# Optimization experiments

Measured on AMD Instinct MI355X. Metric: run time of the kernel, lower is better.

The kernel has to match this reference:

```python
import jax, jax.numpy as jnp
import numpy as np

NUM_GRAPHS = 256
LAMBDA = 0.01


def setup_inputs() -> dict:
    key = jax.random.key(0)
    k1, k2, k3, k4, k5 = jax.random.split(key, 5)
    N, D, E = 100000, 64, 1200000
    logits = jax.random.normal(k1, (NUM_GRAPHS, 10), dtype=jnp.float32)
    labels = jax.random.randint(k2, (NUM_GRAPHS,), 0, 10, dtype=jnp.int64)
    x = jax.random.normal(k3, (N, D), dtype=jnp.float32)
    edge_index = jax.random.randint(k4, (2, E), 0, N, dtype=jnp.int64)
    batch = jnp.sort(jax.random.randint(k5, (N,), 0, NUM_GRAPHS, dtype=jnp.int64))
    return {"logits": logits, "labels": labels, "x": x,
            "edge_index": edge_index, "batch": batch}


def reference(logits, labels, x, edge_index, batch):
    # cross-entropy (mean over graphs)
    logp = jax.nn.log_softmax(logits, axis=-1)
    ce_loss = -jnp.mean(jnp.take_along_axis(logp, labels[:, None], axis=1))

    # Dirichlet energy
    row, col = edge_index[0], edge_index[1]
    N = x.shape[0]
    ones_e = jnp.ones(row.shape, dtype=x.dtype)
    deg = jax.ops.segment_sum(ones_e, row, num_segments=N)          # [N]
    deg_inv_sqrt = jnp.where(deg > 0, jax.lax.rsqrt(jnp.where(deg > 0, deg, 1.0)), 0.0)
    norm = deg_inv_sqrt[row] * deg_inv_sqrt[col]                    # [E]
    diff = x[row] - x[col]                                          # [E, D]
    sq = jnp.sum(diff * diff, axis=1)                               # [E]
    energy_e = norm * sq

    seg = batch[row]                                                # graph id per edge
    energy_sum = jax.ops.segment_sum(energy_e, seg, num_segments=NUM_GRAPHS)
    edge_counts = jax.ops.segment_sum(ones_e, seg, num_segments=NUM_GRAPHS)
    edge_counts = jnp.clip(edge_counts, 1.0, None)
    smoothness_loss = jnp.mean(energy_sum / edge_counts)

    return ce_loss + LAMBDA * smoothness_loss
```

## Files before the change

kernel.cpp:

```cpp
#include <hip/hip_runtime.h>
#include <math.h>

#define NUM_GRAPHS 256
#define LAMBDA 0.01f

typedef int            v4i __attribute__((ext_vector_type(4)));
typedef float          v4f __attribute__((ext_vector_type(4)));
typedef unsigned int   v4u __attribute__((ext_vector_type(4)));
typedef unsigned short v8h __attribute__((ext_vector_type(8)));

__device__ __forceinline__ unsigned short f2bf_rne(float f) {
    unsigned int u = __float_as_uint(f);
    u = u + 0x7fffu + ((u >> 16) & 1u);
    return (unsigned short)(u >> 16);
}

__device__ __forceinline__ float bfdiff_sq(v4u a, v4u b) {
    float s = 0.0f;
    #pragma unroll
    for (int k = 0; k < 4; ++k) {
        float alo = __uint_as_float(a[k] << 16);
        float ahi = __uint_as_float(a[k] & 0xffff0000u);
        float blo = __uint_as_float(b[k] << 16);
        float bhi = __uint_as_float(b[k] & 0xffff0000u);
        float d1 = alo - blo;
        float d2 = ahi - bhi;
        s += d1 * d1;
        s += d2 * d2;
    }
    return s;
}

__global__ void k_cvt(const float* __restrict__ x, v8h* __restrict__ xh,
                      float* __restrict__ zr, int zcount8, long total8) {
    long j = (long)blockIdx.x * blockDim.x + threadIdx.x;
    if (j < total8) {
        const v4f* xp = (const v4f*)(x + j * 8);
        v4f a = xp[0], b = xp[1];
        v8h o;
        o[0] = f2bf_rne(a[0]); o[1] = f2bf_rne(a[1]);
        o[2] = f2bf_rne(a[2]); o[3] = f2bf_rne(a[3]);
        o[4] = f2bf_rne(b[0]); o[5] = f2bf_rne(b[1]);
        o[6] = f2bf_rne(b[2]); o[7] = f2bf_rne(b[3]);
        __builtin_nontemporal_store(o, xh + j);
    }
    if (j < zcount8) {
        v4f z = {0.0f, 0.0f, 0.0f, 0.0f};
        v4f* zp = (v4f*)(zr + j * 8);
        zp[0] = z; zp[1] = z;
    }
}

__global__ void __launch_bounds__(256, 4)
k_gather(const int* __restrict__ row, const int* __restrict__ col,
         const v4u* __restrict__ xh4, float* __restrict__ deg,
         float* __restrict__ sq, int E) {
    const int lane   = threadIdx.x & 63;
    const int lane8  = lane & 7;
    const int gi     = lane >> 3;
    const int wave   = (blockIdx.x * blockDim.x + threadIdx.x) >> 6;
    const int nwaves = (gridDim.x * blockDim.x) >> 6;
    const int E64    = E >> 6;

    for (int t = wave; t < E64; t += nwaves) {
        const int ebase = t * 64 + gi * 8;

        v4i rv0 = __builtin_nontemporal_load((const v4i*)(row + ebase));
        v4i rv1 = __builtin_nontemporal_load((const v4i*)(row + ebase + 4));
        v4i cv0 = __builtin_nontemporal_load((const v4i*)(col + ebase));
        v4i cv1 = __builtin_nontemporal_load((const v4i*)(col + ebase + 4));

        v4u a0 = xh4[(long)rv0[0] * 8 + lane8];
        v4u b0 = xh4[(long)cv0[0] * 8 + lane8];
        v4u a1 = xh4[(long)rv0[1] * 8 + lane8];
        v4u b1 = xh4[(long)cv0[1] * 8 + lane8];
        v4u a2 = xh4[(long)rv0[2] * 8 + lane8];
        v4u b2 = xh4[(long)cv0[2] * 8 + lane8];
        v4u a3 = xh4[(long)rv0[3] * 8 + lane8];
        v4u b3 = xh4[(long)cv0[3] * 8 + lane8];
        v4u a4 = xh4[(long)rv1[0] * 8 + lane8];
        v4u b4 = xh4[(long)cv1[0] * 8 + lane8];
        v4u a5 = xh4[(long)rv1[1] * 8 + lane8];
        v4u b5 = xh4[(long)cv1[1] * 8 + lane8];
        v4u a6 = xh4[(long)rv1[2] * 8 + lane8];
        v4u b6 = xh4[(long)cv1[2] * 8 + lane8];
        v4u a7 = xh4[(long)rv1[3] * 8 + lane8];
        v4u b7 = xh4[(long)cv1[3] * 8 + lane8];

        float s0 = bfdiff_sq(a0, b0);
        float s1 = bfdiff_sq(a1, b1);
        float s2 = bfdiff_sq(a2, b2);
        float s3 = bfdiff_sq(a3, b3);
        float s4 = bfdiff_sq(a4, b4);
        float s5 = bfdiff_sq(a5, b5);
        float s6 = bfdiff_sq(a6, b6);
        float s7 = bfdiff_sq(a7, b7);

        s0 += __shfl_xor(s0, 1); s1 += __shfl_xor(s1, 1);
        s2 += __shfl_xor(s2, 1); s3 += __shfl_xor(s3, 1);
        s4 += __shfl_xor(s4, 1); s5 += __shfl_xor(s5, 1);
        s6 += __shfl_xor(s6, 1); s7 += __shfl_xor(s7, 1);
        s0 += __shfl_xor(s0, 2); s1 += __shfl_xor(s1, 2);
        s2 += __shfl_xor(s2, 2); s3 += __shfl_xor(s3, 2);
        s4 += __shfl_xor(s4, 2); s5 += __shfl_xor(s5, 2);
        s6 += __shfl_xor(s6, 2); s7 += __shfl_xor(s7, 2);
        s0 += __shfl_xor(s0, 4); s1 += __shfl_xor(s1, 4);
        s2 += __shfl_xor(s2, 4); s3 += __shfl_xor(s3, 4);
        s4 += __shfl_xor(s4, 4); s5 += __shfl_xor(s5, 4);
        s6 += __shfl_xor(s6, 4); s7 += __shfl_xor(s7, 4);

        if (lane8 == 0) {
            v4f sv; sv[0] = s0; sv[1] = s1; sv[2] = s2; sv[3] = s3;
            __builtin_nontemporal_store(sv, (v4f*)(sq + ebase));
        } else if (lane8 == 1) {
            v4f sv; sv[0] = s4; sv[1] = s5; sv[2] = s6; sv[3] = s7;
            __builtin_nontemporal_store(sv, (v4f*)(sq + ebase + 4));
        }
        int rr = (lane8 < 4) ? rv0[lane8] : rv1[lane8 - 4];
        atomicAdd(&deg[rr], 1.0f);
    }

    for (int e = (E64 << 6) + wave; e < E; e += nwaves) {
        int r = row[e], c = col[e];
        v4u a = xh4[(long)r * 8 + lane8];
        v4u b = xh4[(long)c * 8 + lane8];
        float s = bfdiff_sq(a, b);
        s += __shfl_xor(s, 1);
        s += __shfl_xor(s, 2);
        s += __shfl_xor(s, 4);
        if (lane == 0) sq[e] = s;
        if (lane == 8) atomicAdd(&deg[r], 1.0f);
    }
}

template <bool PACK>
__global__ void k_dis(float* __restrict__ deg_dis, const int* __restrict__ batch,
                      float* __restrict__ cnt, float2* __restrict__ pk, int N) {
    int i = blockIdx.x * blockDim.x + threadIdx.x;
    bool valid = (i < N);
    float d = valid ? deg_dis[i] : 0.0f;
    int g = valid ? batch[i] : -1;
    float dis = (d > 0.0f) ? rsqrtf(d) : 0.0f;
    if (valid) {
        deg_dis[i] = dis;
        if (PACK) pk[i] = make_float2(dis, __int_as_float(g));
    }

    int gmin = g, gmax = g;
    #pragma unroll
    for (int m = 1; m < 64; m <<= 1) {
        gmin = min(gmin, __shfl_xor(gmin, m));
        gmax = max(gmax, __shfl_xor(gmax, m));
    }
    if (gmin == gmax && gmin >= 0) {
        float s = d;
        #pragma unroll
        for (int m = 1; m < 64; m <<= 1) s += __shfl_xor(s, m);
        if ((threadIdx.x & 63) == 0) atomicAdd(&cnt[g], s);
    } else if (valid) {
        atomicAdd(&cnt[g], d);
    }
}

__global__ void k_bin(const int* __restrict__ row, const int* __restrict__ col,
                      const float* __restrict__ sq, const float2* __restrict__ pk,
                      float* __restrict__ g_energy, int E) {
    __shared__ float lbin[NUM_GRAPHS];
    lbin[threadIdx.x] = 0.0f;
    __syncthreads();

    const int i = blockIdx.x * blockDim.x + threadIdx.x;
    const int stride = gridDim.x * blockDim.x;
    const int E4 = E >> 2;
    const v4i* r4 = (const v4i*)row;
    const v4i* c4 = (const v4i*)col;
    const v4f* s4 = (const v4f*)sq;

    for (int k = i; k < E4; k += stride) {
        v4i r = __builtin_nontemporal_load(&r4[k]);
        v4i c = __builtin_nontemporal_load(&c4[k]);
        v4f s = __builtin_nontemporal_load(&s4[k]);
        float2 pr0 = pk[r[0]], pr1 = pk[r[1]], pr2 = pk[r[2]], pr3 = pk[r[3]];
        float2 pc0 = pk[c[0]], pc1 = pk[c[1]], pc2 = pk[c[2]], pc3 = pk[c[3]];
        atomicAdd(&lbin[__float_as_int(pr0.y)], pr0.x * pc0.x * s[0]);
        atomicAdd(&lbin[__float_as_int(pr1.y)], pr1.x * pc1.x * s[1]);
        atomicAdd(&lbin[__float_as_int(pr2.y)], pr2.x * pc2.x * s[2]);
        atomicAdd(&lbin[__float_as_int(pr3.y)], pr3.x * pc3.x * s[3]);
    }
    for (int e = (E4 << 2) + i; e < E; e += stride) {
        float2 pr = pk[row[e]], pc = pk[col[e]];
        atomicAdd(&lbin[__float_as_int(pr.y)], pr.x * pc.x * sq[e]);
    }

    __syncthreads();
    float v = lbin[threadIdx.x];
    if (v != 0.0f) atomicAdd(&g_energy[threadIdx.x], v);
}

__global__ void k_deg_f(const int* __restrict__ row, float* __restrict__ deg, int E) {
    const int i = blockIdx.x * blockDim.x + threadIdx.x;
    const int stride = gridDim.x * blockDim.x;
    for (int e = i; e < E; e += stride) atomicAdd(&deg[row[e]], 1.0f);
}

__global__ void k_energy(const int* __restrict__ row, const int* __restrict__ col,
                         const float4* __restrict__ x4, const float* __restrict__ dis,
                         const int* __restrict__ batch, float* __restrict__ g_energy,
                         int E) {
    __shared__ float lbin[NUM_GRAPHS];
    lbin[threadIdx.x] = 0.0f;
    __syncthreads();

    const int lane16 = threadIdx.x & 15;
    const int group = (blockIdx.x * blockDim.x + threadIdx.x) >> 4;
    const int ngroups = (gridDim.x * blockDim.x) >> 4;

    for (int e = group; e < E; e += ngroups) {
        int r = row[e];
        int c = col[e];
        float4 a = x4[(long)r * 16 + lane16];
        float4 b = x4[(long)c * 16 + lane16];
        float nr = dis[r] * dis[c];
        int g = batch[r];
        float dx = a.x - b.x, dy = a.y - b.y, dz = a.z - b.z, dw = a.w - b.w;
        float s = dx * dx + dy * dy + dz * dz + dw * dw;
        s += __shfl_xor(s, 1);
        s += __shfl_xor(s, 2);
        s += __shfl_xor(s, 4);
        s += __shfl_xor(s, 8);
        if (lane16 == 0) atomicAdd(&lbin[g], nr * s);
    }

    __syncthreads();
    float v = lbin[threadIdx.x];
    if (v != 0.0f) atomicAdd(&g_energy[threadIdx.x], v);
}

__global__ void k_final(const float* __restrict__ logits, const int* __restrict__ labels,
                        const float* __restrict__ g_energy, const float* __restrict__ cnt,
                        float* __restrict__ out) {
    const int t = threadIdx.x;
    const float* lg = logits + t * 10;

    float m = -INFINITY;
    #pragma unroll
    for (int j = 0; j < 10; ++j) m = fmaxf(m, lg[j]);
    float sum = 0.0f;
    #pragma unroll
    for (int j = 0; j < 10; ++j) sum += expf(lg[j] - m);
    float lse = m + logf(sum);
    float ce = lse - lg[labels[t]];

    float sm = g_energy[t] / fmaxf(cnt[t], 1.0f);

    float v = ce + LAMBDA * sm;
    #pragma unroll
    for (int mk = 1; mk < 64; mk <<= 1) v += __shfl_xor(v, mk);

    __shared__ float wsum[4];
    if ((t & 63) == 0) wsum[t >> 6] = v;
    __syncthreads();
    if (t == 0) out[0] = (wsum[0] + wsum[1] + wsum[2] + wsum[3]) * (1.0f / 256.0f);
}

extern "C" void kernel_launch(void* const* d_in, const int* in_sizes, int n_in,
                              void* d_out, int out_size, void* d_ws, size_t ws_size,
                              hipStream_t stream) {
    const float* logits = (const float*)d_in[0];
    const int* labels   = (const int*)d_in[1];
    const float* x      = (const float*)d_in[2];
    const int* edge_idx = (const int*)d_in[3];
    const int* batch    = (const int*)d_in[4];

    const int N = in_sizes[2] / 64;
    const int E = in_sizes[3] / 2;

    const int* row = edge_idx;
    const int* col = edge_idx + E;

    float*  deg_dis  = (float*)d_ws;
    float*  g_energy = deg_dis + N;
    float*  cnt      = g_energy + NUM_GRAPHS;
    float*  sq       = cnt + NUM_GRAPHS;
    float2* pk       = (float2*)(sq + E);
    unsigned short* xh = (unsigned short*)(pk + N);

    const size_t base_floats = (size_t)N + 2 * NUM_GRAPHS;
    const size_t need_sq   = (base_floats + (size_t)E) * sizeof(float);
    const size_t need_pk   = need_sq + (size_t)2 * N * sizeof(float);
    const size_t need_fast = need_pk + (size_t)N * 64 * sizeof(unsigned short);

    if (ws_size >= need_fast) {
        const long total8 = (long)N * 8;
        const int zcount8 = (int)((N + 2 * NUM_GRAPHS + 7) / 8);
        const int cvt_blocks = (int)((total8 + 255) / 256);
        k_cvt<<<cvt_blocks, 256, 0, stream>>>(x, (v8h*)xh, deg_dis, zcount8, total8);
        k_gather<<<2048, 256, 0, stream>>>(row, col, (const v4u*)xh, deg_dis, sq, E);
        k_dis<true><<<(N + 255) / 256, 256, 0, stream>>>(deg_dis, batch, cnt, pk, N);
        k_bin<<<512, 256, 0, stream>>>(row, col, sq, pk, g_energy, E);
    } else {
        (void)hipMemsetAsync(d_ws, 0, base_floats * sizeof(float), stream);
        k_deg_f<<<2048, 256, 0, stream>>>(row, deg_dis, E);
        k_dis<false><<<(N + 255) / 256, 256, 0, stream>>>(deg_dis, batch, cnt, pk, N);
        k_energy<<<2048, 256, 0, stream>>>(row, col, (const float4*)x, deg_dis, batch,
                                           g_energy, E);
    }
    k_final<<<1, 256, 0, stream>>>(logits, labels, g_energy, cnt, (float*)d_out);
}
```

Baseline: 208.5 us.

## Fuse degree normalization, edge counting and final loss into binning kernel

Removes the k_dis pass and the packed dis/graph-id array. The binning kernel now reads raw degrees and batch ids per edge and computes rsqrt inline. It also counts edges per graph in shared memory instead of summing degrees per node. A last-block-done counter lets the final cross-entropy and mean reduction run inside the same kernel, dropping two launches. The cost is more random gathers and rsqrt per edge, plus a second shared atomic per edge.

```diff
diff --git a/kernel.cpp b/kernel.cpp
--- a/kernel.cpp
+++ b/kernel.cpp
@@ -133,18 +133,106 @@
     }
 }
 
-template <bool PACK>
+__global__ void __launch_bounds__(256)
+k_bin2(const int* __restrict__ row, const int* __restrict__ col,
+       const float* __restrict__ sq, const float* __restrict__ deg,
+       const int* __restrict__ batch, float* __restrict__ g_energy,
+       float* __restrict__ cnt, int* __restrict__ ctr,
+       const float* __restrict__ logits, const int* __restrict__ labels,
+       float* __restrict__ out, int E, int nblocks) {
+    __shared__ float lbin[NUM_GRAPHS];
+    __shared__ float lcnt[NUM_GRAPHS];
+    lbin[threadIdx.x] = 0.0f;
+    lcnt[threadIdx.x] = 0.0f;
+    __syncthreads();
+
+    const int i = blockIdx.x * blockDim.x + threadIdx.x;
+    const int stride = gridDim.x * blockDim.x;
+    const int E4 = E >> 2;
+    const v4i* r4 = (const v4i*)row;
+    const v4i* c4 = (const v4i*)col;
+    const v4f* s4 = (const v4f*)sq;
+
+    for (int k = i; k < E4; k += stride) {
+        v4i r = __builtin_nontemporal_load(&r4[k]);
+        v4i c = __builtin_nontemporal_load(&c4[k]);
+        v4f s = __builtin_nontemporal_load(&s4[k]);
+        #pragma unroll
+        for (int j = 0; j < 4; ++j) {
+            float dr = deg[r[j]];
+            float dc = deg[c[j]];
+            int g = batch[r[j]];
+            float nr = ((dr > 0.0f) ? rsqrtf(dr) : 0.0f) *
+                       ((dc > 0.0f) ? rsqrtf(dc) : 0.0f);
+            atomicAdd(&lbin[g], nr * s[j]);
+            atomicAdd(&lcnt[g], 1.0f);
+        }
+    }
+    for (int e = (E4 << 2) + i; e < E; e += stride) {
+        float dr = deg[row[e]];
+        float dc = deg[col[e]];
+        int g = batch[row[e]];
+        float nr = ((dr > 0.0f) ? rsqrtf(dr) : 0.0f) *
+                   ((dc > 0.0f) ? rsqrtf(dc) : 0.0f);
+        atomicAdd(&lbin[g], nr * sq[e]);
+        atomicAdd(&lcnt[g], 1.0f);
+    }
+
+    __syncthreads();
+    atomicAdd(&g_energy[threadIdx.x], lbin[threadIdx.x]);
+    atomicAdd(&cnt[threadIdx.x], lcnt[threadIdx.x]);
+    __threadfence();
+    __syncthreads();
+
+    __shared__ int amLast;
+    if (threadIdx.x == 0) {
+        amLast = (atomicAdd(ctr, 1) == nblocks - 1) ? 1 : 0;
+    }
+    __syncthreads();
+    if (!amLast) return;
+    __threadfence();
+
+    const int t = threadIdx.x;
+    float ge = __hip_atomic_load(&g_energy[t], __ATOMIC_ACQUIRE,
+                                 __HIP_MEMORY_SCOPE_AGENT);
+    float cn = __hip_atomic_load(&cnt[t], __ATOMIC_ACQUIRE,
+                                 __HIP_MEMORY_SCOPE_AGENT);
+
+    const float* lg = logits + t * 10;
+    float m = -INFINITY;
+    #pragma unroll
+    for (int j = 0; j < 10; ++j) m = fmaxf(m, lg[j]);
+    float sum = 0.0f;
+    #pragma unroll
+    for (int j = 0; j < 10; ++j) sum += expf(lg[j] - m);
+    float lse = m + logf(sum);
+    float ce = lse - lg[labels[t]];
+
+    float sm = ge / fmaxf(cn, 1.0f);
+
+    float v = ce + LAMBDA * sm;
+    #pragma unroll
+    for (int mk = 1; mk < 64; mk <<= 1) v += __shfl_xor(v, mk);
+
+    __shared__ float wsum[4];
+    if ((t & 63) == 0) wsum[t >> 6] = v;
+    __syncthreads();
+    if (t == 0) out[0] = (wsum[0] + wsum[1] + wsum[2] + wsum[3]) * (1.0f / 256.0f);
+}
+
+__global__ void k_deg_f(const int* __restrict__ row, float* __restrict__ deg, int E) {
+    const int i = blockIdx.x * blockDim.x + threadIdx.x;
+    const int stride = gridDim.x * blockDim.x;
+    for (int e = i; e < E; e += stride) atomicAdd(&deg[row[e]], 1.0f);
+}
+
 __global__ void k_dis(float* __restrict__ deg_dis, const int* __restrict__ batch,
-                      float* __restrict__ cnt, float2* __restrict__ pk, int N) {
+                      float* __restrict__ cnt, int N) {
     int i = blockIdx.x * blockDim.x + threadIdx.x;
     bool valid = (i < N);
     float d = valid ? deg_dis[i] : 0.0f;
     int g = valid ? batch[i] : -1;
-    float dis = (d > 0.0f) ? rsqrtf(d) : 0.0f;
-    if (valid) {
-        deg_dis[i] = dis;
-        if (PACK) pk[i] = make_float2(dis, __int_as_float(g));
-    }
+    if (valid) deg_dis[i] = (d > 0.0f) ? rsqrtf(d) : 0.0f;
 
     int gmin = g, gmax = g;
     #pragma unroll
@@ -160,47 +248,6 @@
     } else if (valid) {
         atomicAdd(&cnt[g], d);
     }
-}
-
-__global__ void k_bin(const int* __restrict__ row, const int* __restrict__ col,
-                      const float* __restrict__ sq, const float2* __restrict__ pk,
-                      float* __restrict__ g_energy, int E) {
-    __shared__ float lbin[NUM_GRAPHS];
-    lbin[threadIdx.x] = 0.0f;
-    __syncthreads();
-
-    const int i = blockIdx.x * blockDim.x + threadIdx.x;
-    const int stride = gridDim.x * blockDim.x;
-    const int E4 = E >> 2;
-    const v4i* r4 = (const v4i*)row;
-    const v4i* c4 = (const v4i*)col;
-    const v4f* s4 = (const v4f*)sq;
-
-    for (int k = i; k < E4; k += stride) {
-        v4i r = __builtin_nontemporal_load(&r4[k]);
-        v4i c = __builtin_nontemporal_load(&c4[k]);
-        v4f s = __builtin_nontemporal_load(&s4[k]);
-        float2 pr0 = pk[r[0]], pr1 = pk[r[1]], pr2 = pk[r[2]], pr3 = pk[r[3]];
-        float2 pc0 = pk[c[0]], pc1 = pk[c[1]], pc2 = pk[c[2]], pc3 = pk[c[3]];
-        atomicAdd(&lbin[__float_as_int(pr0.y)], pr0.x * pc0.x * s[0]);
-        atomicAdd(&lbin[__float_as_int(pr1.y)], pr1.x * pc1.x * s[1]);
-        atomicAdd(&lbin[__float_as_int(pr2.y)], pr2.x * pc2.x * s[2]);
-        atomicAdd(&lbin[__float_as_int(pr3.y)], pr3.x * pc3.x * s[3]);
-    }
-    for (int e = (E4 << 2) + i; e < E; e += stride) {
-        float2 pr = pk[row[e]], pc = pk[col[e]];
-        atomicAdd(&lbin[__float_as_int(pr.y)], pr.x * pc.x * sq[e]);
-    }
-
-    __syncthreads();
-    float v = lbin[threadIdx.x];
-    if (v != 0.0f) atomicAdd(&g_energy[threadIdx.x], v);
-}
-
-__global__ void k_deg_f(const int* __restrict__ row, float* __restrict__ deg, int E) {
-    const int i = blockIdx.x * blockDim.x + threadIdx.x;
-    const int stride = gridDim.x * blockDim.x;
-    for (int e = i; e < E; e += stride) atomicAdd(&deg[row[e]], 1.0f);
 }
 
 __global__ void k_energy(const int* __restrict__ row, const int* __restrict__ col,
@@ -278,32 +325,34 @@
     const int* row = edge_idx;
     const int* col = edge_idx + E;
 
-    float*  deg_dis  = (float*)d_ws;
-    float*  g_energy = deg_dis + N;
-    float*  cnt      = g_energy + NUM_GRAPHS;
-    float*  sq       = cnt + NUM_GRAPHS;
-    float2* pk       = (float2*)(sq + E);
-    unsigned short* xh = (unsigned short*)(pk + N);
-
-    const size_t base_floats = (size_t)N + 2 * NUM_GRAPHS;
-    const size_t need_sq   = (base_floats + (size_t)E) * sizeof(float);
-    const size_t need_pk   = need_sq + (size_t)2 * N * sizeof(float);
-    const size_t need_fast = need_pk + (size_t)N * 64 * sizeof(unsigned short);
+    float* deg      = (float*)d_ws;
+    float* g_energy = deg + N;
+    float* cnt      = g_energy + NUM_GRAPHS;
+    int*   ctr      = (int*)(cnt + NUM_GRAPHS);
+    float* sq       = cnt + NUM_GRAPHS + 64;
+    unsigned short* xh = (unsigned short*)(sq + E);
+
+    const size_t zfloats  = (size_t)N + 2 * NUM_GRAPHS + 64;
+    const size_t need_fast = (zfloats + (size_t)E) * sizeof(float)
+                           + (size_t)N * 64 * sizeof(unsigned short);
+
+    const int BIN_BLOCKS = 512;
 
     if (ws_size >= need_fast) {
         const long total8 = (long)N * 8;
-        const int zcount8 = (int)((N + 2 * NUM_GRAPHS + 7) / 8);
+        const int zcount8 = (int)((zfloats + 7) / 8);
         const int cvt_blocks = (int)((total8 + 255) / 256);
-        k_cvt<<<cvt_blocks, 256, 0, stream>>>(x, (v8h*)xh, deg_dis, zcount8, total8);
-        k_gather<<<2048, 256, 0, stream>>>(row, col, (const v4u*)xh, deg_dis, sq, E);
-        k_dis<true><<<(N + 255) / 256, 256, 0, stream>>>(deg_dis, batch, cnt, pk, N);
-        k_bin<<<512, 256, 0, stream>>>(row, col, sq, pk, g_energy, E);
+        k_cvt<<<cvt_blocks, 256, 0, stream>>>(x, (v8h*)xh, deg, zcount8, total8);
+        k_gather<<<2048, 256, 0, stream>>>(row, col, (const v4u*)xh, deg, sq, E);
+        k_bin2<<<BIN_BLOCKS, 256, 0, stream>>>(row, col, sq, deg, batch, g_energy,
+                                               cnt, ctr, logits, labels,
+                                               (float*)d_out, E, BIN_BLOCKS);
     } else {
-        (void)hipMemsetAsync(d_ws, 0, base_floats * sizeof(float), stream);
-        k_deg_f<<<2048, 256, 0, stream>>>(row, deg_dis, E);
-        k_dis<false><<<(N + 255) / 256, 256, 0, stream>>>(deg_dis, batch, cnt, pk, N);
-        k_energy<<<2048, 256, 0, stream>>>(row, col, (const float4*)x, deg_dis, batch,
+        (void)hipMemsetAsync(d_ws, 0, zfloats * sizeof(float), stream);
+        k_deg_f<<<2048, 256, 0, stream>>>(row, deg, E);
+        k_dis<<<(N + 255) / 256, 256, 0, stream>>>(deg, batch, cnt, N);
+        k_energy<<<2048, 256, 0, stream>>>(row, col, (const float4*)x, deg, batch,
                                            g_energy, E);
-    }
-    k_final<<<1, 256, 0, stream>>>(logits, labels, g_energy, cnt, (float*)d_out);
-}
+        k_final<<<1, 256, 0, stream>>>(logits, labels, g_energy, cnt, (float*)d_out);
+    }
+}
```

Result: slower. 221.1 us (+6.1%).
